# Kernel optimization log

Measured on AMD Instinct MI355X. Metric: run time of the kernel, lower is better.

Reference implementation:

```python
import jax, jax.numpy as jnp
import numpy as np

B, N, D = 2, 2048, 1024
H, WS = 16, 128  # num_heads, window_size
DH = D // H
HALF = WS // 2  # window is [i-HALF, i+HALF] inclusive -> 129 keys interior


def setup_inputs() -> dict:
    key = jax.random.key(0)
    ks = jax.random.split(key, 5)
    return {
        "x": jax.random.normal(ks[0], (B, N, D), dtype=jnp.float32),
        "Wqkv": jax.random.normal(ks[1], (D, 3 * D), dtype=jnp.float32) * 0.02,
        "bqkv": jax.random.normal(ks[2], (3 * D,), dtype=jnp.float32) * 0.02,
        "Wout": jax.random.normal(ks[3], (D, D), dtype=jnp.float32) * 0.02,
        "bout": jax.random.normal(ks[4], (D,), dtype=jnp.float32) * 0.02,
    }


def reference(x, Wqkv, bqkv, Wout, bout):
    b, n, d = x.shape
    scale = DH ** -0.5
    qkv = x @ Wqkv + bqkv  # [b, n, 3d]
    q, k, v = jnp.split(qkv, 3, axis=-1)
    # [b, n, d] -> [b, h, n, dh]
    def heads(t):
        return t.reshape(b, n, H, DH).transpose(0, 2, 1, 3)
    q, k, v = heads(q), heads(k), heads(v)
    scores = jnp.einsum("bhid,bhjd->bhij", q, k) * scale  # [b, h, n, n]
    # per-token window [max(0,i-HALF), min(n,i+HALF+1)) == |i-j| <= HALF
    idx = jnp.arange(n)
    band = jnp.abs(idx[:, None] - idx[None, :]) <= HALF  # [n, n]
    neg = jnp.asarray(jnp.finfo(scores.dtype).min, scores.dtype)
    scores = jnp.where(band[None, None], scores, neg)
    attn = jax.nn.softmax(scores, axis=-1)
    out = jnp.einsum("bhij,bhjd->bhid", attn, v)  # [b, h, n, dh]
    out = out.transpose(0, 2, 1, 3).reshape(b, n, d)
    return out @ Wout + bout
```

## Files before the change

### kernel.cpp

```cpp
#include <hip/hip_runtime.h>
#include <hip/hip_bf16.h>
#include <cstdint>
#include <cstddef>

#define BB 2
#define NN 2048
#define DD 1024
#define HH 16
#define DHH 64
#define SCALE 0.125f

typedef _Float16 f16x8 __attribute__((ext_vector_type(8)));
typedef _Float16 f16x4 __attribute__((ext_vector_type(4)));
typedef float f32x4 __attribute__((ext_vector_type(4)));

#define AS1(p) ((__attribute__((address_space(1))) void*)(p))
#define AS3(p) ((__attribute__((address_space(3))) void*)(p))

__global__ __launch_bounds__(256) void prep(const float* __restrict__ x, _Float16* __restrict__ x_h,
                                            const float* __restrict__ Wqkv, _Float16* __restrict__ Wqkv_t,
                                            const float* __restrict__ Wout, _Float16* __restrict__ Wout_t) {
    __shared__ float tile[32][33];
    int bx = blockIdx.x, tid = threadIdx.x;
    if (bx < 2048) {
        int i = bx * 2048 + tid * 8;
        f32x4 a = *(const f32x4*)(x + i);
        f32x4 b = *(const f32x4*)(x + i + 4);
        f16x8 o;
        o[0] = (_Float16)a[0]; o[1] = (_Float16)a[1]; o[2] = (_Float16)a[2]; o[3] = (_Float16)a[3];
        o[4] = (_Float16)b[0]; o[5] = (_Float16)b[1]; o[6] = (_Float16)b[2]; o[7] = (_Float16)b[3];
        *(f16x8*)(x_h + i) = o;
        return;
    }
    const float* in; _Float16* out; int C, tc, tr;
    if (bx < 5120) { int t = bx - 2048; C = 3 * DD; in = Wqkv; out = Wqkv_t; tc = t % 96; tr = t / 96; }
    else           { int t = bx - 5120; C = DD;     in = Wout; out = Wout_t; tc = t % 32; tr = t / 32; }
    int R = DD;
    int txx = tid & 31, ty = tid >> 5;
    int r0 = tr * 32, c0 = tc * 32;
#pragma unroll
    for (int i = 0; i < 32; i += 8)
        tile[ty + i][txx] = in[(size_t)(r0 + ty + i) * C + (c0 + txx)];
    __syncthreads();
#pragma unroll
    for (int i = 0; i < 32; i += 8)
        out[(size_t)(c0 + ty + i) * R + (r0 + txx)] = (_Float16)tile[txx][ty + i];
}

template <bool SWAP, int MT>
__device__ __forceinline__ void gemm_kloop(const _Float16* __restrict__ gA,
                                           const _Float16* __restrict__ gB,
                                           _Float16* lA, _Float16* lB,
                                           const _Float16* As, const _Float16* Bs,
                                           int wm, int wn, int llo, int lhi, int K,
                                           f32x4 acc[][MT > 4 ? MT : 4]) {
    for (int k0 = 0; k0 < K; k0 += 64) {
        __syncthreads();
#pragma unroll
        for (int p = 0; p < MT; ++p)
            __builtin_amdgcn_global_load_lds(AS1(gA + (size_t)p * 8 * K + k0), AS3(lA + p * 512), 16, 0, 0);
#pragma unroll
        for (int p = 0; p < 4; ++p)
            __builtin_amdgcn_global_load_lds(AS1(gB + (size_t)p * 8 * K + k0), AS3(lB + p * 512), 16, 0, 0);
        __syncthreads();

#pragma unroll
        for (int ks = 0; ks < 2; ++ks) {
            f16x8 af[MT], bf[4];
            int swz = (((ks * 4 + lhi) ^ (llo & 7)) * 8);
#pragma unroll
            for (int mt = 0; mt < MT; ++mt)
                af[mt] = *(const f16x8*)(As + (wm + mt * 16 + llo) * 64 + swz);
#pragma unroll
            for (int nt = 0; nt < 4; ++nt)
                bf[nt] = *(const f16x8*)(Bs + (wn + nt * 16 + llo) * 64 + swz);
            if (SWAP) {
#pragma unroll
                for (int nt = 0; nt < 4; ++nt)
#pragma unroll
                    for (int mt = 0; mt < MT; ++mt)
                        acc[nt][mt] = __builtin_amdgcn_mfma_f32_16x16x32_f16(bf[nt], af[mt], acc[nt][mt], 0, 0, 0);
            } else {
#pragma unroll
                for (int mt = 0; mt < MT; ++mt)
#pragma unroll
                    for (int nt = 0; nt < 4; ++nt)
                        acc[mt][nt] = __builtin_amdgcn_mfma_f32_16x16x32_f16(af[mt], bf[nt], acc[mt][nt], 0, 0, 0);
            }
        }
    }
}

__global__ __launch_bounds__(256) void gemm_qkv(const _Float16* __restrict__ A,
                                                const _Float16* __restrict__ Bt,
                                                const float* __restrict__ bias,
                                                _Float16* __restrict__ q_h,
                                                _Float16* __restrict__ k_h,
                                                _Float16* __restrict__ vt_h) {
    const int K = DD;
    __shared__ __align__(16) _Float16 As[128 * 64];
    __shared__ __align__(16) _Float16 Bs[128 * 64];
    int id = blockIdx.x;
    int xcd = id & 7, j = id >> 3;
    int bn = (xcd * 3 + j % 3) * 128;
    int bm = (j / 3) * 128;
    int tid = threadIdx.x;
    int wave = tid >> 6, lane = tid & 63;
    int wm = (wave >> 1) * 64, wn = (wave & 1) * 64;
    int lhi = lane >> 4, llo = lane & 15;

    f32x4 acc[4][4] = {};

    int srow = wave * 32 + (lane >> 3);
    int scol = ((lane & 7) ^ (lane >> 3)) * 8;
    const _Float16* gA = A + (size_t)(bm + srow) * K + scol;
    const _Float16* gB = Bt + (size_t)(bn + srow) * K + scol;
    _Float16* lA = As + wave * 2048 + lane * 8;
    _Float16* lB = Bs + wave * 2048 + lane * 8;

    int region = bn >> 10;
    if (region == 2) {
        gemm_kloop<false, 4>(gA, gB, lA, lB, As, Bs, wm, wn, llo, lhi, K, acc);
#pragma unroll
        for (int nt = 0; nt < 4; ++nt) {
            int col = bn + wn + nt * 16 + llo;
            float bv = bias[col];
            int c = col & 1023;
            int h = c >> 6, dh = c & 63;
#pragma unroll
            for (int mt = 0; mt < 4; ++mt) {
                int row = bm + wm + mt * 16 + lhi * 4;
                int b = row >> 11, n = row & 2047;
                f16x4 v4;
#pragma unroll
                for (int r = 0; r < 4; ++r) v4[r] = (_Float16)(acc[mt][nt][r] + bv);
                *(f16x4*)(vt_h + ((size_t)((b * HH + h) * DHH + dh)) * NN + n) = v4;
            }
        }
    } else {
        gemm_kloop<true, 4>(gA, gB, lA, lB, As, Bs, wm, wn, llo, lhi, K, acc);
        _Float16* dst0 = (region == 0 ? q_h : k_h);
#pragma unroll
        for (int nt = 0; nt < 4; ++nt) {
            int cbase = bn + wn + nt * 16 + lhi * 4;
            f32x4 b4 = *(const f32x4*)(bias + cbase);
            int c = cbase & 1023;
#pragma unroll
            for (int mt = 0; mt < 4; ++mt) {
                int t = bm + wm + mt * 16 + llo;
                int b = t >> 11, n = t & 2047;
                f16x4 v4;
#pragma unroll
                for (int r = 0; r < 4; ++r) v4[r] = (_Float16)(acc[nt][mt][r] + b4[r]);
                *(f16x4*)(dst0 + (size_t)(b * NN + n) * DD + c) = v4;
            }
        }
    }
}

__global__ __launch_bounds__(256) void gemm_out(const _Float16* __restrict__ A,
                                                const _Float16* __restrict__ Bt,
                                                const float* __restrict__ bias,
                                                float* __restrict__ Cf) {
    const int K = DD, N = DD;
    __shared__ __align__(16) _Float16 As[64 * 64];
    __shared__ __align__(16) _Float16 Bs[128 * 64];
    int id = blockIdx.x;
    int xcd = id & 7, j = id >> 3;
    int bm = (xcd * 8 + (j >> 3)) * 64;
    int bn = (j & 7) * 128;
    int tid = threadIdx.x;
    int wave = tid >> 6, lane = tid & 63;
    int wm = (wave >> 1) * 32, wn = (wave & 1) * 64;
    int lhi = lane >> 4, llo = lane & 15;

    f32x4 acc[4][4] = {};

    int srowA = wave * 16 + (lane >> 3);
    int srowB = wave * 32 + (lane >> 3);
    int scol = ((lane & 7) ^ (lane >> 3)) * 8;
    const _Float16* gA = A + (size_t)(bm + srowA) * K + scol;
    const _Float16* gB = Bt + (size_t)(bn + srowB) * K + scol;
    _Float16* lA = As + wave * 1024 + lane * 8;
    _Float16* lB = Bs + wave * 2048 + lane * 8;

    gemm_kloop<true, 2>(gA, gB, lA, lB, As, Bs, wm, wn, llo, lhi, K,
                        (f32x4(*)[4])acc);

#pragma unroll
    for (int nt = 0; nt < 4; ++nt) {
        int cbase = bn + wn + nt * 16 + lhi * 4;
        f32x4 b4 = *(const f32x4*)(bias + cbase);
#pragma unroll
        for (int mt = 0; mt < 2; ++mt) {
            int t = bm + wm + mt * 16 + llo;
            f32x4 v4;
#pragma unroll
            for (int r = 0; r < 4; ++r) v4[r] = acc[nt][mt][r] + b4[r];
            *(f32x4*)(Cf + (size_t)t * N + cbase) = v4;
        }
    }
}

#define KP 64
#define PP 200
#define VP 200
__global__ __launch_bounds__(256) void local_attn(const _Float16* __restrict__ q_h,
                                                  const _Float16* __restrict__ k_h,
                                                  const _Float16* __restrict__ vt_h,
                                                  _Float16* __restrict__ outh) {
    __shared__ __align__(16) _Float16 KsPs[64 * PP];
    __shared__ __align__(16) _Float16 Vt[64 * VP];
    _Float16* Ks = KsPs;
    _Float16* Ps = KsPs;
    int tid = threadIdx.x;
    int id = blockIdx.x;
    int xcd = id & 7, j = id >> 3;
    int i0 = (xcd * 4 + (j & 3)) * 64;
    int hb = j >> 2;
    int h = hb & 15, b = hb >> 4;

    int wave = tid >> 6, lane = tid & 63;
    int llo = lane & 15, lhi = lane >> 4;

    {
        int srow = lane >> 3;
        int chunk = ((lane & 7) ^ (lane >> 3)) * 8;
        const _Float16* kb = k_h + (size_t)(b * NN) * DD + h * DHH + chunk;
#pragma unroll
        for (int q = 0; q < 6; ++q) {
            int p = wave * 6 + q;
            int jj = i0 - 64 + p * 8 + srow;
            __builtin_amdgcn_global_load_lds(AS1(kb + (ptrdiff_t)jj * DD), AS3(Ks + p * 512 + lane * 8), 16, 0, 0);
        }
    }

    {
        const _Float16* vb = vt_h + (size_t)((b * HH + h) * DHH) * NN + (i0 - 64);
        for (int u = tid; u < 1536; u += 256) {
            int d = u / 24, c = u % 24;
            f16x8 vv = *(const f16x8*)(vb + (ptrdiff_t)d * NN + c * 8);
            *(f16x8*)(Vt + d * VP + c * 8) = vv;
        }
    }

    int qrow = wave * 16 + llo;
    int qi = i0 + qrow;
    const _Float16* qp = q_h + (size_t)(b * NN + qi) * DD + h * DHH;
    f16x8 qf0 = *(const f16x8*)(qp + lhi * 8);
    f16x8 qf1 = *(const f16x8*)(qp + 32 + lhi * 8);
    __syncthreads();

    float sc[12][4];
#pragma unroll
    for (int mt = 0; mt < 12; ++mt) {
        const _Float16* kr = Ks + (mt * 16 + llo) * 64;
        f16x8 kf0 = *(const f16x8*)(kr + ((lhi ^ (llo & 7)) * 8));
        f16x8 kf1 = *(const f16x8*)(kr + (((lhi + 4) ^ (llo & 7)) * 8));
        f32x4 a = {0.f, 0.f, 0.f, 0.f};
        a = __builtin_amdgcn_mfma_f32_16x16x32_f16(kf0, qf0, a, 0, 0, 0);
        a = __builtin_amdgcn_mfma_f32_16x16x32_f16(kf1, qf1, a, 0, 0, 0);
#pragma unroll
        for (int r = 0; r < 4; ++r) sc[mt][r] = a[r];
    }
    __syncthreads();

    float m = -1e30f;
#pragma unroll
    for (int mt = 0; mt < 12; ++mt)
#pragma unroll
        for (int r = 0; r < 4; ++r) {
            int sidx = mt * 16 + lhi * 4 + r;
            int jj = i0 - 64 + sidx;
            int dj = jj - qi;
            bool valid = (jj >= 0) && (jj < NN) && (dj <= 64) && (dj >= -64);
            float v = valid ? sc[mt][r] * SCALE : -1e30f;
            sc[mt][r] = v;
            m = fmaxf(m, v);
        }
    m = fmaxf(m, __shfl_xor(m, 16, 64));
    m = fmaxf(m, __shfl_xor(m, 32, 64));
    float l = 0.f;
#pragma unroll
    for (int mt = 0; mt < 12; ++mt)
#pragma unroll
        for (int r = 0; r < 4; ++r) {
            float e = __expf(sc[mt][r] - m);
            sc[mt][r] = e;
            l += e;
        }
    l += __shfl_xor(l, 16, 64);
    l += __shfl_xor(l, 32, 64);
    float invl = 1.f / l;

#pragma unroll
    for (int mt = 0; mt < 12; ++mt) {
        f16x4 pv;
#pragma unroll
        for (int r = 0; r < 4; ++r) pv[r] = (_Float16)(sc[mt][r] * invl);
        *(f16x4*)(Ps + qrow * PP + mt * 16 + lhi * 4) = pv;
    }
    __asm__ volatile("s_waitcnt lgkmcnt(0)" ::: "memory");

    f32x4 oacc[4] = {};
#pragma unroll
    for (int ks = 0; ks < 6; ++ks) {
        f16x8 pf = *(const f16x8*)(Ps + (wave * 16 + llo) * PP + ks * 32 + lhi * 8);
#pragma unroll
        for (int nt = 0; nt < 4; ++nt) {
            f16x8 vf = *(const f16x8*)(Vt + (nt * 16 + llo) * VP + ks * 32 + lhi * 8);
            oacc[nt] = __builtin_amdgcn_mfma_f32_16x16x32_f16(pf, vf, oacc[nt], 0, 0, 0);
        }
    }

    _Float16* orow = outh + (size_t)(b * NN) * DD + h * DHH;
#pragma unroll
    for (int nt = 0; nt < 4; ++nt)
#pragma unroll
        for (int r = 0; r < 4; ++r) {
            int q = wave * 16 + lhi * 4 + r;
            int d = nt * 16 + llo;
            orow[(size_t)(i0 + q) * DD + d] = (_Float16)oacc[nt][r];
        }
}

extern "C" void kernel_launch(void* const* d_in, const int* in_sizes, int n_in,
                              void* d_out, int out_size, void* d_ws, size_t ws_size,
                              hipStream_t stream) {
    const float* x    = (const float*)d_in[0];
    const float* Wqkv = (const float*)d_in[1];
    const float* bqkv = (const float*)d_in[2];
    const float* Wout = (const float*)d_in[3];
    const float* bout = (const float*)d_in[4];
    float* out = (float*)d_out;

    char* ws = (char*)d_ws;
    _Float16* x_h    = (_Float16*)(ws);
    _Float16* Wqkv_t = (_Float16*)(ws + (size_t)8  * 1024 * 1024);
    _Float16* Wout_t = (_Float16*)(ws + (size_t)14 * 1024 * 1024);
    _Float16* q_h    = (_Float16*)(ws + (size_t)16 * 1024 * 1024);
    _Float16* k_h    = (_Float16*)(ws + (size_t)24 * 1024 * 1024);
    _Float16* vt_h   = (_Float16*)(ws + (size_t)32 * 1024 * 1024);
    _Float16* attn_h = (_Float16*)(ws + (size_t)40 * 1024 * 1024);

    prep<<<6144, 256, 0, stream>>>(x, x_h, Wqkv, Wqkv_t, Wout, Wout_t);

    gemm_qkv<<<768, 256, 0, stream>>>(x_h, Wqkv_t, bqkv, q_h, k_h, vt_h);

    local_attn<<<1024, 256, 0, stream>>>(q_h, k_h, vt_h, attn_h);

    gemm_out<<<512, 256, 0, stream>>>(attn_h, Wout_t, bout, out);
}
```

Measured before the change: 155.9 us.

## Rewrite QKV GEMM with 256x256 tiles, 8 waves, and interleaved double-buffered pipeline

Replaces the 128x128 QKV GEMM, which ran 768 blocks of 4 waves, with 256x256 tiles run by 192 blocks of 8 waves. It double-buffers LDS via global_load_lds and splits each k-step into four quarter phases that interleave loads with MFMA, using s_setprio around the MFMA bursts. The larger tile raises arithmetic intensity and the schedule aims to hide global-load latency behind compute. The cost is 128KB of LDS per block, heavier register use, and only 192 blocks, which may underfill the 256 CUs.

```diff
diff --git a/kernel.cpp b/kernel.cpp
--- a/kernel.cpp
+++ b/kernel.cpp
@@ -91,36 +91,163 @@
     }
 }
 
-__global__ __launch_bounds__(256) void gemm_qkv(const _Float16* __restrict__ A,
-                                                const _Float16* __restrict__ Bt,
-                                                const float* __restrict__ bias,
-                                                _Float16* __restrict__ q_h,
-                                                _Float16* __restrict__ k_h,
-                                                _Float16* __restrict__ vt_h) {
-    const int K = DD;
-    __shared__ __align__(16) _Float16 As[128 * 64];
-    __shared__ __align__(16) _Float16 Bs[128 * 64];
-    int id = blockIdx.x;
-    int xcd = id & 7, j = id >> 3;
-    int bn = (xcd * 3 + j % 3) * 128;
-    int bm = (j / 3) * 128;
+template <bool SWAP>
+__device__ __forceinline__ void qkv_body(const _Float16* __restrict__ A,
+                                         const _Float16* __restrict__ Bt,
+                                         const float* __restrict__ bias,
+                                         _Float16* __restrict__ q_h,
+                                         _Float16* __restrict__ k_h,
+                                         _Float16* __restrict__ vt_h,
+                                         _Float16* As, _Float16* Bs,
+                                         int bm, int bn, int region) {
+    (void)region;
     int tid = threadIdx.x;
     int wave = tid >> 6, lane = tid & 63;
-    int wm = (wave >> 1) * 64, wn = (wave & 1) * 64;
-    int lhi = lane >> 4, llo = lane & 15;
-
-    f32x4 acc[4][4] = {};
-
-    int srow = wave * 32 + (lane >> 3);
-    int scol = ((lane & 7) ^ (lane >> 3)) * 8;
-    const _Float16* gA = A + (size_t)(bm + srow) * K + scol;
-    const _Float16* gB = Bt + (size_t)(bn + srow) * K + scol;
-    _Float16* lA = As + wave * 2048 + lane * 8;
-    _Float16* lB = Bs + wave * 2048 + lane * 8;
-
-    int region = bn >> 10;
-    if (region == 2) {
-        gemm_kloop<false, 4>(gA, gB, lA, lB, As, Bs, wm, wn, llo, lhi, K, acc);
+    int llo = lane & 15, lhi = lane >> 4;
+    int wm = (wave >> 2) * 128, wn = (wave & 3) * 64;
+    int l8 = lane >> 3;
+    int gchunk = ((lane & 7) ^ l8) * 8;
+
+    int rAu = wm + (wave & 3) * 16;
+    int rBu = (wave >> 1) * 64 + (wave & 1) * 16;
+    const _Float16* gA = A + (size_t)(bm + rAu + l8) * DD + gchunk;
+    const _Float16* gB = Bt + (size_t)(bn + rBu + l8) * DD + gchunk;
+    _Float16* lA = As + rAu * 64 + lane * 8;
+    _Float16* lB = Bs + rBu * 64 + lane * 8;
+
+#define STA(H, C, T, U) __builtin_amdgcn_global_load_lds( \
+        AS1(gA + (size_t)((H) * 64 + (C) * 8) * DD + (T) * 64), \
+        AS3(lA + (U) * 16384 + ((H) * 64 + (C) * 8) * 64), 16, 0, 0)
+#define STB(H, C, T, U) __builtin_amdgcn_global_load_lds( \
+        AS1(gB + (size_t)((H) * 32 + (C) * 8) * DD + (T) * 64), \
+        AS3(lB + (U) * 16384 + ((H) * 32 + (C) * 8) * 64), 16, 0, 0)
+#define RDA(MT, KS, U) (*(const f16x8*)(As + (U) * 16384 + (wm + (MT) * 16 + llo) * 64 + ((((KS) * 4 + lhi) ^ (llo & 7)) * 8)))
+#define RDB(NT, KS, U) (*(const f16x8*)(Bs + (U) * 16384 + (wn + (NT) * 16 + llo) * 64 + ((((KS) * 4 + lhi) ^ (llo & 7)) * 8)))
+#define MM(MT, NT, KS) do { \
+        if constexpr (SWAP) acc[NT][MT] = __builtin_amdgcn_mfma_f32_16x16x32_f16(bf[NT][KS], af[(MT) & 3][KS], acc[NT][MT], 0, 0, 0); \
+        else acc[MT][NT] = __builtin_amdgcn_mfma_f32_16x16x32_f16(af[(MT) & 3][KS], bf[NT][KS], acc[MT][NT], 0, 0, 0); \
+    } while (0)
+
+    f32x4 acc[SWAP ? 4 : 8][SWAP ? 8 : 4] = {};
+    f16x8 af[4][2], bf[4][2];
+
+    STA(0, 0, 0, 0); STA(0, 1, 0, 0);
+    STB(0, 0, 0, 0); STB(0, 1, 0, 0);
+    STB(1, 0, 0, 0); STB(1, 1, 0, 0);
+    STA(1, 0, 0, 0); STA(1, 1, 0, 0);
+    asm volatile("s_waitcnt vmcnt(4)" ::: "memory");
+    __builtin_amdgcn_s_barrier();
+
+#pragma unroll 1
+    for (int t = 0; t < 15; ++t) {
+        int u = t & 1, nu = u ^ 1;
+#pragma unroll
+        for (int mt = 0; mt < 4; ++mt) { af[mt][0] = RDA(mt, 0, u); af[mt][1] = RDA(mt, 1, u); }
+#pragma unroll
+        for (int nt = 0; nt < 2; ++nt) { bf[nt][0] = RDB(nt, 0, u); bf[nt][1] = RDB(nt, 1, u); }
+        STA(0, 0, t + 1, nu); STA(0, 1, t + 1, nu);
+        __builtin_amdgcn_s_barrier();
+        asm volatile("s_waitcnt lgkmcnt(0)" ::: "memory");
+        __builtin_amdgcn_s_setprio(1);
+#pragma unroll
+        for (int ks = 0; ks < 2; ++ks)
+#pragma unroll
+            for (int mt = 0; mt < 4; ++mt) { MM(mt, 0, ks); MM(mt, 1, ks); }
+        __builtin_amdgcn_s_setprio(0);
+        asm volatile("s_waitcnt vmcnt(4)" ::: "memory");
+        __builtin_amdgcn_s_barrier();
+#pragma unroll
+        for (int nt = 2; nt < 4; ++nt) { bf[nt][0] = RDB(nt, 0, u); bf[nt][1] = RDB(nt, 1, u); }
+        STB(0, 0, t + 1, nu); STB(0, 1, t + 1, nu);
+        __builtin_amdgcn_s_barrier();
+        asm volatile("s_waitcnt lgkmcnt(0)" ::: "memory");
+        __builtin_amdgcn_s_setprio(1);
+#pragma unroll
+        for (int ks = 0; ks < 2; ++ks)
+#pragma unroll
+            for (int mt = 0; mt < 4; ++mt) { MM(mt, 2, ks); MM(mt, 3, ks); }
+        __builtin_amdgcn_s_setprio(0);
+        asm volatile("s_waitcnt vmcnt(4)" ::: "memory");
+        __builtin_amdgcn_s_barrier();
+#pragma unroll
+        for (int mt = 0; mt < 4; ++mt) { af[mt][0] = RDA(mt + 4, 0, u); af[mt][1] = RDA(mt + 4, 1, u); }
+        STB(1, 0, t + 1, nu); STB(1, 1, t + 1, nu);
+        __builtin_amdgcn_s_barrier();
+        asm volatile("s_waitcnt lgkmcnt(0)" ::: "memory");
+        __builtin_amdgcn_s_setprio(1);
+#pragma unroll
+        for (int ks = 0; ks < 2; ++ks)
+#pragma unroll
+            for (int mt = 4; mt < 8; ++mt) { MM(mt, 2, ks); MM(mt, 3, ks); }
+        __builtin_amdgcn_s_setprio(0);
+        __builtin_amdgcn_s_barrier();
+        STA(1, 0, t + 1, nu); STA(1, 1, t + 1, nu);
+        __builtin_amdgcn_s_barrier();
+        __builtin_amdgcn_s_setprio(1);
+#pragma unroll
+        for (int ks = 0; ks < 2; ++ks)
+#pragma unroll
+            for (int mt = 4; mt < 8; ++mt) { MM(mt, 0, ks); MM(mt, 1, ks); }
+        __builtin_amdgcn_s_setprio(0);
+        asm volatile("s_waitcnt vmcnt(4)" ::: "memory");
+        __builtin_amdgcn_s_barrier();
+    }
+
+    {
+#pragma unroll
+        for (int mt = 0; mt < 4; ++mt) { af[mt][0] = RDA(mt, 0, 1); af[mt][1] = RDA(mt, 1, 1); }
+#pragma unroll
+        for (int nt = 0; nt < 2; ++nt) { bf[nt][0] = RDB(nt, 0, 1); bf[nt][1] = RDB(nt, 1, 1); }
+        __builtin_amdgcn_s_barrier();
+        asm volatile("s_waitcnt lgkmcnt(0)" ::: "memory");
+        __builtin_amdgcn_s_setprio(1);
+#pragma unroll
+        for (int ks = 0; ks < 2; ++ks)
+#pragma unroll
+            for (int mt = 0; mt < 4; ++mt) { MM(mt, 0, ks); MM(mt, 1, ks); }
+        __builtin_amdgcn_s_setprio(0);
+        asm volatile("s_waitcnt vmcnt(2)" ::: "memory");
+        __builtin_amdgcn_s_barrier();
+#pragma unroll
+        for (int nt = 2; nt < 4; ++nt) { bf[nt][0] = RDB(nt, 0, 1); bf[nt][1] = RDB(nt, 1, 1); }
+        asm volatile("s_waitcnt lgkmcnt(0)" ::: "memory");
+        __builtin_amdgcn_s_setprio(1);
+#pragma unroll
+        for (int ks = 0; ks < 2; ++ks)
+#pragma unroll
+            for (int mt = 0; mt < 4; ++mt) { MM(mt, 2, ks); MM(mt, 3, ks); }
+        __builtin_amdgcn_s_setprio(0);
+        asm volatile("s_waitcnt vmcnt(0)" ::: "memory");
+        __builtin_amdgcn_s_barrier();
+#pragma unroll
+        for (int mt = 0; mt < 4; ++mt) { af[mt][0] = RDA(mt + 4, 0, 1); af[mt][1] = RDA(mt + 4, 1, 1); }
+        asm volatile("s_waitcnt lgkmcnt(0)" ::: "memory");
+        __builtin_amdgcn_s_setprio(1);
+#pragma unroll
+        for (int ks = 0; ks < 2; ++ks)
+#pragma unroll
+            for (int mt = 4; mt < 8; ++mt) { MM(mt, 0, ks); MM(mt, 1, ks); MM(mt, 2, ks); MM(mt, 3, ks); }
+        __builtin_amdgcn_s_setprio(0);
+    }
+
+    if constexpr (SWAP) {
+        _Float16* dst0 = (region == 0 ? q_h : k_h);
+#pragma unroll
+        for (int nt = 0; nt < 4; ++nt) {
+            int cbase = bn + wn + nt * 16 + lhi * 4;
+            f32x4 b4 = *(const f32x4*)(bias + cbase);
+            int c = cbase & 1023;
+#pragma unroll
+            for (int mt = 0; mt < 8; ++mt) {
+                int tkn = bm + wm + mt * 16 + llo;
+                int b = tkn >> 11, n = tkn & 2047;
+                f16x4 v4;
+#pragma unroll
+                for (int r = 0; r < 4; ++r) v4[r] = (_Float16)(acc[nt][mt][r] + b4[r]);
+                *(f16x4*)(dst0 + (size_t)(b * NN + n) * DD + c) = v4;
+            }
+        }
+    } else {
 #pragma unroll
         for (int nt = 0; nt < 4; ++nt) {
             int col = bn + wn + nt * 16 + llo;
@@ -128,7 +255,7 @@
             int c = col & 1023;
             int h = c >> 6, dh = c & 63;
 #pragma unroll
-            for (int mt = 0; mt < 4; ++mt) {
+            for (int mt = 0; mt < 8; ++mt) {
                 int row = bm + wm + mt * 16 + lhi * 4;
                 int b = row >> 11, n = row & 2047;
                 f16x4 v4;
@@ -137,25 +264,32 @@
                 *(f16x4*)(vt_h + ((size_t)((b * HH + h) * DHH + dh)) * NN + n) = v4;
             }
         }
-    } else {
-        gemm_kloop<true, 4>(gA, gB, lA, lB, As, Bs, wm, wn, llo, lhi, K, acc);
-        _Float16* dst0 = (region == 0 ? q_h : k_h);
-#pragma unroll
-        for (int nt = 0; nt < 4; ++nt) {
-            int cbase = bn + wn + nt * 16 + lhi * 4;
-            f32x4 b4 = *(const f32x4*)(bias + cbase);
-            int c = cbase & 1023;
-#pragma unroll
-            for (int mt = 0; mt < 4; ++mt) {
-                int t = bm + wm + mt * 16 + llo;
-                int b = t >> 11, n = t & 2047;
-                f16x4 v4;
-#pragma unroll
-                for (int r = 0; r < 4; ++r) v4[r] = (_Float16)(acc[nt][mt][r] + b4[r]);
-                *(f16x4*)(dst0 + (size_t)(b * NN + n) * DD + c) = v4;
-            }
-        }
-    }
+    }
+#undef STA
+#undef STB
+#undef RDA
+#undef RDB
+#undef MM
+}
+
+__global__ __launch_bounds__(512, 2) void gemm_qkv(const _Float16* __restrict__ A,
+                                                   const _Float16* __restrict__ Bt,
+                                                   const float* __restrict__ bias,
+                                                   _Float16* __restrict__ q_h,
+                                                   _Float16* __restrict__ k_h,
+                                                   _Float16* __restrict__ vt_h) {
+    __shared__ __align__(16) _Float16 As[2 * 16384];
+    __shared__ __align__(16) _Float16 Bs[2 * 16384];
+    int id = blockIdx.x;
+    int xcd = id & 7, jj = id >> 3;
+    int mtile = (xcd >> 1) * 4 + jj / 6;
+    int ntile = (xcd & 1) * 6 + jj % 6;
+    int bm = mtile * 256, bn = ntile * 256;
+    int region = bn >> 10;
+    if (region == 2)
+        qkv_body<false>(A, Bt, bias, q_h, k_h, vt_h, As, Bs, bm, bn, region);
+    else
+        qkv_body<true>(A, Bt, bias, q_h, k_h, vt_h, As, Bs, bm, bn, region);
 }
 
 __global__ __launch_bounds__(256) void gemm_out(const _Float16* __restrict__ A,
@@ -345,7 +479,7 @@
 
     prep<<<6144, 256, 0, stream>>>(x, x_h, Wqkv, Wqkv_t, Wout, Wout_t);
 
-    gemm_qkv<<<768, 256, 0, stream>>>(x_h, Wqkv_t, bqkv, q_h, k_h, vt_h);
+    gemm_qkv<<<192, 512, 0, stream>>>(x_h, Wqkv_t, bqkv, q_h, k_h, vt_h);
 
     local_attn<<<1024, 256, 0, stream>>>(q_h, k_h, vt_h, attn_h);
 
```

New measurement: 154.8 us. No clear change (-0.7%).
